# Kernel optimization log

Measured on AMD Instinct MI355X. Metric: run time of the kernel, lower is better.

The kernel has to match this reference:

```python
import jax, jax.numpy as jnp
import numpy as np

BATCH, SEQ, D_MODEL, N_HEADS, D_HEAD = 2, 2048, 2048, 16, 128
ATTN_SCALE = np.sqrt(D_HEAD).astype(np.float32)
IGNORE = jnp.float32(-1e5)


def setup_inputs() -> dict:
    key = jax.random.key(0)
    ks = jax.random.split(key, 5)
    init = 1.0 / np.sqrt(D_MODEL)
    return {
        "x": jax.random.normal(ks[0], (BATCH, SEQ, D_MODEL), jnp.float32),
        "W_Q": jax.random.normal(ks[1], (N_HEADS, D_MODEL, D_HEAD), jnp.float32) * init,
        "W_K": jax.random.normal(ks[2], (N_HEADS, D_MODEL, D_HEAD), jnp.float32) * init,
        "W_V": jax.random.normal(ks[3], (N_HEADS, D_MODEL, D_HEAD), jnp.float32) * init,
        "W_O": jax.random.normal(ks[4], (N_HEADS, D_HEAD, D_MODEL), jnp.float32) * init,
        "b_Q": jnp.zeros((N_HEADS, D_HEAD), jnp.float32),
        "b_K": jnp.zeros((N_HEADS, D_HEAD), jnp.float32),
        "b_V": jnp.zeros((N_HEADS, D_HEAD), jnp.float32),
        "b_O": jnp.zeros((D_MODEL,), jnp.float32),
    }


def reference(x, W_Q, W_K, W_V, W_O, b_Q, b_K, b_V, b_O):
    # q,k,v: [batch, pos, head, d_head]
    q = jnp.einsum('bpd,hde->bphe', x, W_Q) + b_Q
    k = jnp.einsum('bpd,hde->bphe', x, W_K) + b_K
    v = jnp.einsum('bpd,hde->bphe', x, W_V) + b_V
    # scores: [batch, head, query_pos, key_pos]
    scores = jnp.einsum('bqhe,bkhe->bhqk', q, k) / ATTN_SCALE
    S = x.shape[1]
    causal = jnp.tril(jnp.ones((S, S), bool))
    scores = jnp.where(causal, scores, IGNORE)
    attn = jax.nn.softmax(scores, axis=-1)
    z = jnp.einsum('bkhe,bhqk->bqhe', v, attn)
    out = jnp.einsum('bqhe,hed->bqd', z, W_O) + b_O
    return out
```

## Files before the change

### kernel.cpp

```cpp
#include <hip/hip_runtime.h>

typedef unsigned int uint;
typedef unsigned short ushort;
typedef __bf16 bf16x8 __attribute__((ext_vector_type(8)));
typedef float f32x4 __attribute__((ext_vector_type(4)));
typedef uint u32x4 __attribute__((ext_vector_type(4)));

#define DEV static __device__ __forceinline__

#define BATCH 2
#define SEQ 2048
#define DMODEL 2048
#define NHEADS 16
#define DHEAD 128
#define MROWS (BATCH*SEQ)
#define RSCALE 0.08838834764831845f
#define LOG2E  1.4426950408889634f

DEV float fast_exp2(float x) { return __builtin_amdgcn_exp2f(x); }

DEV bf16x8 as_frag(u32x4 v) { return __builtin_bit_cast(bf16x8, v); }
DEV ushort f2bf(float f) {
  uint u = __builtin_bit_cast(uint, f);
  u += 0x7fffu + ((u >> 16) & 1u);
  return (ushort)(u >> 16);
}
DEV u32x4 lds_ld16(const ushort* p) { return *(const u32x4*)p; }

DEV void async_cp16(const ushort* g, ushort* l) {
  __builtin_amdgcn_global_load_lds(
      (const __attribute__((address_space(1))) uint*)g,
      (__attribute__((address_space(3))) uint*)l, 16, 0, 0);
}

__global__ __launch_bounds__(256) void prep(
    const float* __restrict__ x,
    const float* __restrict__ Wq, const float* __restrict__ Wk,
    const float* __restrict__ Wv, const float* __restrict__ Wo,
    ushort* __restrict__ xb, ushort* __restrict__ WqT,
    ushort* __restrict__ WkT, ushort* __restrict__ WvT,
    ushort* __restrict__ WoT)
{
  int id = blockIdx.x;
  if (id < 8192) {
    int i = id * 256 + threadIdx.x;
    float4 v = ((const float4*)x)[i];
    union { ushort u[4]; uint2 w; } o;
    o.u[0] = f2bf(v.x); o.u[1] = f2bf(v.y); o.u[2] = f2bf(v.z); o.u[3] = f2bf(v.w);
    ((uint2*)xb)[i] = o.w;
    return;
  }
  __shared__ ushort t[32][33];
  id -= 8192;
  const float* src; ushort* dst; int R, C, c0, r0;
  if (id < 12288) {
    int which = id >> 12;
    int r = id & 4095;
    int slice = r >> 8;
    int rem = r & 255;
    int ty = rem >> 2, tx = rem & 3;
    const float* S[3] = {Wq, Wk, Wv};
    ushort* D[3] = {WqT, WkT, WvT};
    src = S[which] + (size_t)slice * DMODEL * DHEAD;
    dst = D[which] + (size_t)slice * DMODEL * DHEAD;
    R = DMODEL; C = DHEAD; c0 = tx * 32; r0 = ty * 32;
  } else {
    id -= 12288;
    int tx = id & 63, ty = id >> 6;
    src = Wo; dst = WoT; R = DMODEL; C = DMODEL; c0 = tx * 32; r0 = ty * 32;
  }
  int xx = threadIdx.x & 31, yy = threadIdx.x >> 5;
  #pragma unroll
  for (int i = 0; i < 32; i += 8)
    t[yy + i][xx] = f2bf(src[(size_t)(r0 + yy + i) * C + (c0 + xx)]);
  __syncthreads();
  #pragma unroll
  for (int i = 0; i < 32; i += 8)
    dst[(size_t)(c0 + yy + i) * R + (r0 + xx)] = t[xx][yy + i];
}

__global__ __launch_bounds__(256, 4) void gemm_qkv(
    const ushort* __restrict__ xb,
    const ushort* __restrict__ WqT, const ushort* __restrict__ WkT,
    const ushort* __restrict__ WvT,
    const float* __restrict__ bQ, const float* __restrict__ bK,
    const float* __restrict__ bV,
    ushort* __restrict__ Qo, ushort* __restrict__ Ko, ushort* __restrict__ Vt)
{
  int mt = blockIdx.x;
  int h  = blockIdx.y;
  int which = blockIdx.z;
  const ushort* Bt = (which == 0) ? WqT : (which == 1) ? WkT : WvT;
  const float* bias = (which == 0) ? bQ : (which == 1) ? bK : bV;
  Bt += (size_t)h * DHEAD * DMODEL;
  bias += h * DHEAD;

  __shared__ __align__(16) ushort As[128 * 64];
  __shared__ __align__(16) ushort Bs[128 * 64];

  int tid = threadIdx.x, lane = tid & 63, w = tid >> 6;
  int wm = w >> 1, wn = w & 1;
  int l16 = lane & 15, quad = lane >> 4;

  const ushort* Ag = xb + (size_t)(mt * 128) * DMODEL;

  int soff[4]; int sc[4];
  #pragma unroll
  for (int t = 0; t < 4; t++) {
    int c = w * 4 + t;
    int r = c * 8 + (lane >> 3);
    int p = lane & 7;
    int g = p ^ (r & 7);
    soff[t] = r * DMODEL + g * 8;
    sc[t] = c * 512;
  }

  f32x4 acc[4][4] = {};

  for (int k0 = 0; k0 < DMODEL; k0 += 64) {
    __syncthreads();
    #pragma unroll
    for (int t = 0; t < 4; t++) {
      async_cp16(Ag + soff[t] + k0, As + sc[t]);
      async_cp16(Bt + soff[t] + k0, Bs + sc[t]);
    }
    __syncthreads();
    #pragma unroll
    for (int kk = 0; kk < 2; kk++) {
      bf16x8 a[4], b[4];
      #pragma unroll
      for (int i = 0; i < 4; i++) {
        int row = wm * 64 + i * 16 + l16;
        int p = (kk * 4 + quad) ^ (l16 & 7);
        a[i] = as_frag(lds_ld16(As + row * 64 + p * 8));
      }
      #pragma unroll
      for (int i = 0; i < 4; i++) {
        int row = wn * 64 + i * 16 + l16;
        int p = (kk * 4 + quad) ^ (l16 & 7);
        b[i] = as_frag(lds_ld16(Bs + row * 64 + p * 8));
      }
      #pragma unroll
      for (int i = 0; i < 4; i++)
        #pragma unroll
        for (int j = 0; j < 4; j++)
          acc[i][j] = __builtin_amdgcn_mfma_f32_16x16x32_bf16(a[i], b[j], acc[i][j], 0, 0, 0);
    }
  }

  float scale = (which == 0) ? RSCALE * LOG2E : 1.0f;
  #pragma unroll
  for (int i = 0; i < 4; i++) {
    #pragma unroll
    for (int j = 0; j < 4; j++) {
      int col = wn * 64 + j * 16 + l16;
      float bb = bias[col];
      #pragma unroll
      for (int r = 0; r < 4; r++) {
        int row = mt * 128 + wm * 64 + i * 16 + quad * 4 + r;
        int b_ = row >> 11, p = row & 2047;
        int bh = b_ * NHEADS + h;
        ushort val = f2bf((acc[i][j][r] + bb) * scale);
        if (which == 2) {
          Vt[((size_t)bh * DHEAD + col) * SEQ + p] = val;
        } else {
          ushort* Out = (which == 0) ? Qo : Ko;
          Out[((size_t)bh * SEQ + p) * DHEAD + col] = val;
        }
      }
    }
  }
}

__global__ __launch_bounds__(256, 2) void flash_attn(
    const ushort* __restrict__ Q, const ushort* __restrict__ K,
    const ushort* __restrict__ Vt, ushort* __restrict__ Z)
{
  int a  = blockIdx.x;
  int bh = blockIdx.y;
  const ushort* Qg = Q + (size_t)bh * SEQ * DHEAD;
  const ushort* Kg = K + (size_t)bh * SEQ * DHEAD;
  const ushort* Vg = Vt + (size_t)bh * DHEAD * SEQ;

  __shared__ __align__(16) ushort Ks[2][64 * 128];
  __shared__ __align__(16) ushort Vs[2][128 * 64];
  __shared__ __align__(16) ushort Ps[64 * 72];

  int tid = threadIdx.x, lane = tid & 63, w = tid >> 6;
  int l16 = lane & 15, quad = lane >> 4;

  int kOff[4], vOff[4], cLds[4];
  #pragma unroll
  for (int t = 0; t < 4; t++) {
    int c = w * 4 + t;
    cLds[t] = c * 512;
    int rk = c * 4 + (lane >> 4);
    int pk = lane & 15;
    int gk = (pk & 8) | ((pk & 7) ^ (rk & 7));
    kOff[t] = rk * DHEAD + gk * 8;
    int ev = c * 8 + (lane >> 3);
    int pv = lane & 7;
    int gv = pv ^ (ev & 7);
    vOff[t] = ev * SEQ + gv * 8;
  }

  #pragma unroll
  for (int ph = 0; ph < 2; ph++) {
    int qt = ph ? a : (31 - a);
    int q0 = qt * 64;

    bf16x8 qf[4];
    int qrow = q0 + w * 16 + l16;
    #pragma unroll
    for (int kb = 0; kb < 4; kb++)
      qf[kb] = as_frag(*(const u32x4*)(Qg + qrow * DHEAD + kb * 32 + quad * 8));

    float m_i[4], l_i[4];
    #pragma unroll
    for (int i = 0; i < 4; i++) { m_i[i] = -1e30f; l_i[i] = 0.0f; }
    f32x4 zacc[8] = {};

    #pragma unroll
    for (int t = 0; t < 4; t++) {
      async_cp16(Kg + kOff[t], Ks[0] + cLds[t]);
      async_cp16(Vg + vOff[t], Vs[0] + cLds[t]);
    }
    __syncthreads();

    for (int j = 0; j <= qt; j++) {
      int cur = j & 1;
      if (j < qt) {
        int k1 = (j + 1) * 64;
        #pragma unroll
        for (int t = 0; t < 4; t++) {
          async_cp16(Kg + k1 * DHEAD + kOff[t], Ks[cur ^ 1] + cLds[t]);
          async_cp16(Vg + k1 + vOff[t], Vs[cur ^ 1] + cLds[t]);
        }
      }
      const ushort* KsC = Ks[cur];
      const ushort* VsC = Vs[cur];

      f32x4 s[4] = {};
      #pragma unroll
      for (int kb = 0; kb < 4; kb++) {
        #pragma unroll
        for (int n = 0; n < 4; n++) {
          int r = n * 16 + l16;
          int ug = kb * 4 + quad;
          int p = (ug & 8) | ((ug & 7) ^ (r & 7));
          bf16x8 b = as_frag(lds_ld16(KsC + r * 128 + p * 8));
          s[n] = __builtin_amdgcn_mfma_f32_16x16x32_bf16(qf[kb], b, s[n], 0, 0, 0);
        }
      }
      if (j == qt) {
        #pragma unroll
        for (int n = 0; n < 4; n++)
          #pragma unroll
          for (int i = 0; i < 4; i++) {
            int qr = 16 * w + quad * 4 + i;
            int kr = n * 16 + l16;
            if (kr > qr) s[n][i] = -1e30f;
          }
      }
      float mx[4];
      #pragma unroll
      for (int i = 0; i < 4; i++)
        mx[i] = fmaxf(fmaxf(s[0][i], s[1][i]), fmaxf(s[2][i], s[3][i]));
      #pragma unroll
      for (int off = 1; off < 16; off <<= 1)
        #pragma unroll
        for (int i = 0; i < 4; i++)
          mx[i] = fmaxf(mx[i], __shfl_xor(mx[i], off, 64));

      float alpha[4], rsum[4];
      #pragma unroll
      for (int i = 0; i < 4; i++) {
        float mn = fmaxf(m_i[i], mx[i]);
        alpha[i] = fast_exp2(m_i[i] - mn);
        m_i[i] = mn;
        rsum[i] = 0.0f;
      }
      #pragma unroll
      for (int n = 0; n < 4; n++)
        #pragma unroll
        for (int i = 0; i < 4; i++) {
          float p = fast_exp2(s[n][i] - m_i[i]);
          rsum[i] += p;
          int row = 16 * w + quad * 4 + i, col = n * 16 + l16;
          Ps[row * 72 + col] = f2bf(p);
        }
      #pragma unroll
      for (int off = 1; off < 16; off <<= 1)
        #pragma unroll
        for (int i = 0; i < 4; i++)
          rsum[i] += __shfl_xor(rsum[i], off, 64);
      #pragma unroll
      for (int i = 0; i < 4; i++) l_i[i] = l_i[i] * alpha[i] + rsum[i];
      #pragma unroll
      for (int n = 0; n < 8; n++)
        #pragma unroll
        for (int i = 0; i < 4; i++) zacc[n][i] *= alpha[i];

      #pragma unroll
      for (int kk = 0; kk < 2; kk++) {
        bf16x8 af = as_frag(lds_ld16(Ps + (w * 16 + l16) * 72 + (kk * 4 + quad) * 8));
        #pragma unroll
        for (int n = 0; n < 8; n++) {
          int e = n * 16 + l16;
          int ug = kk * 4 + quad;
          int p = ug ^ (e & 7);
          bf16x8 b = as_frag(lds_ld16(VsC + e * 64 + p * 8));
          zacc[n] = __builtin_amdgcn_mfma_f32_16x16x32_bf16(af, b, zacc[n], 0, 0, 0);
        }
      }
      __syncthreads();
    }

    int b_ = bh >> 4, h = bh & 15;
    #pragma unroll
    for (int n = 0; n < 8; n++)
      #pragma unroll
      for (int i = 0; i < 4; i++) {
        int row = q0 + 16 * w + quad * 4 + i;
        int col = h * DHEAD + n * 16 + l16;
        Z[((size_t)(b_ * SEQ + row)) * DMODEL + col] = f2bf(zacc[n][i] / l_i[i]);
      }
  }
}

__global__ __launch_bounds__(256, 4) void gemm_out(
    const ushort* __restrict__ Zin, const ushort* __restrict__ WoT,
    const float* __restrict__ bO, float* __restrict__ out)
{
  int mt = blockIdx.x, ntile = blockIdx.y;
  __shared__ __align__(16) ushort As[128 * 64];
  __shared__ __align__(16) ushort Bs[128 * 64];
  int tid = threadIdx.x, lane = tid & 63, w = tid >> 6;
  int wm = w >> 1, wn = w & 1;
  int l16 = lane & 15, quad = lane >> 4;

  const ushort* Ag = Zin + (size_t)(mt * 128) * DMODEL;
  const ushort* Bg = WoT + (size_t)(ntile * 128) * DMODEL;

  int soff[4]; int sc[4];
  #pragma unroll
  for (int t = 0; t < 4; t++) {
    int c = w * 4 + t;
    int r = c * 8 + (lane >> 3);
    int p = lane & 7;
    int g = p ^ (r & 7);
    soff[t] = r * DMODEL + g * 8;
    sc[t] = c * 512;
  }

  f32x4 acc[4][4] = {};
  for (int k0 = 0; k0 < DMODEL; k0 += 64) {
    __syncthreads();
    #pragma unroll
    for (int t = 0; t < 4; t++) {
      async_cp16(Ag + soff[t] + k0, As + sc[t]);
      async_cp16(Bg + soff[t] + k0, Bs + sc[t]);
    }
    __syncthreads();
    #pragma unroll
    for (int kk = 0; kk < 2; kk++) {
      bf16x8 a[4], b[4];
      #pragma unroll
      for (int i = 0; i < 4; i++) {
        int row = wm * 64 + i * 16 + l16;
        int p = (kk * 4 + quad) ^ (l16 & 7);
        a[i] = as_frag(lds_ld16(As + row * 64 + p * 8));
      }
      #pragma unroll
      for (int i = 0; i < 4; i++) {
        int row = wn * 64 + i * 16 + l16;
        int p = (kk * 4 + quad) ^ (l16 & 7);
        b[i] = as_frag(lds_ld16(Bs + row * 64 + p * 8));
      }
      #pragma unroll
      for (int i = 0; i < 4; i++)
        #pragma unroll
        for (int j = 0; j < 4; j++)
          acc[i][j] = __builtin_amdgcn_mfma_f32_16x16x32_bf16(a[i], b[j], acc[i][j], 0, 0, 0);
    }
  }
  #pragma unroll
  for (int i = 0; i < 4; i++) {
    #pragma unroll
    for (int j = 0; j < 4; j++) {
      int col = ntile * 128 + wn * 64 + j * 16 + l16;
      float bb = bO[col];
      #pragma unroll
      for (int r = 0; r < 4; r++) {
        int row = mt * 128 + wm * 64 + i * 16 + quad * 4 + r;
        out[(size_t)row * DMODEL + col] = acc[i][j][r] + bb;
      }
    }
  }
}

extern "C" void kernel_launch(void* const* d_in, const int* in_sizes, int n_in,
                              void* d_out, int out_size, void* d_ws, size_t ws_size,
                              hipStream_t stream)
{
  const float* x  = (const float*)d_in[0];
  const float* Wq = (const float*)d_in[1];
  const float* Wk = (const float*)d_in[2];
  const float* Wv = (const float*)d_in[3];
  const float* Wo = (const float*)d_in[4];
  const float* bQ = (const float*)d_in[5];
  const float* bK = (const float*)d_in[6];
  const float* bV = (const float*)d_in[7];
  const float* bO = (const float*)d_in[8];
  float* out = (float*)d_out;

  ushort* ws = (ushort*)d_ws;
  const size_t WSZ = (size_t)NHEADS * DHEAD * DMODEL;
  const size_t QSZ = (size_t)BATCH * NHEADS * SEQ * DHEAD;
  ushort* xb  = ws;
  ushort* WqT = xb + (size_t)MROWS * DMODEL;
  ushort* WkT = WqT + WSZ;
  ushort* WvT = WkT + WSZ;
  ushort* WoT = WvT + WSZ;
  ushort* Qb  = WoT + (size_t)DMODEL * DMODEL;
  ushort* Kb  = Qb + QSZ;
  ushort* VtB = Kb + QSZ;
  ushort* Zb  = VtB + QSZ;

  dim3 tb(256);
  prep<<<dim3(24576), tb, 0, stream>>>(x, Wq, Wk, Wv, Wo,
                                       xb, WqT, WkT, WvT, WoT);

  gemm_qkv<<<dim3(32, 16, 3), tb, 0, stream>>>(xb, WqT, WkT, WvT, bQ, bK, bV,
                                               Qb, Kb, VtB);

  flash_attn<<<dim3(16, 32), tb, 0, stream>>>(Qb, Kb, VtB, Zb);

  gemm_out<<<dim3(32, 16), tb, 0, stream>>>(Zb, WoT, bO, out);
}
```

Measured before the change: 375.9 us.

## Rewrite QKV GEMM with 256x256 tiles, 8 waves, and double-buffered async pipeline

The QKV projection GEMM moves from 128x128 tiles with 4 waves and a load-sync-compute loop to 256x256 tiles with 8 waves. The new loop double-buffers half-K slices in LDS, prefetches several stages ahead with explicit vmcnt waits, and raises wave priority around the MFMA bursts. A remapped 1D grid groups blocks across the Q/K/V panels, with a head-spanning epilogue. The aim is to hide global load latency and raise reuse per LDS byte, at the cost of more LDS, more registers and fragile hand-tuned wait counts.

```diff
diff --git a/kernel.cpp b/kernel.cpp
--- a/kernel.cpp
+++ b/kernel.cpp
@@ -79,7 +79,7 @@
     dst[(size_t)(c0 + yy + i) * R + (r0 + xx)] = t[xx][yy + i];
 }
 
-__global__ __launch_bounds__(256, 4) void gemm_qkv(
+__global__ __launch_bounds__(512, 2) void gemm_qkv(
     const ushort* __restrict__ xb,
     const ushort* __restrict__ WqT, const ushort* __restrict__ WkT,
     const ushort* __restrict__ WvT,
@@ -87,85 +87,154 @@
     const float* __restrict__ bV,
     ushort* __restrict__ Qo, ushort* __restrict__ Ko, ushort* __restrict__ Vt)
 {
-  int mt = blockIdx.x;
-  int h  = blockIdx.y;
-  int which = blockIdx.z;
-  const ushort* Bt = (which == 0) ? WqT : (which == 1) ? WkT : WvT;
+  int id = blockIdx.x;
+  int W = (id & 7) * 48 + (id >> 3);
+  int which = W >> 7;
+  int rem = W & 127;
+  int nt = rem >> 4;
+  int mt = rem & 15;
+
+  const ushort* Bpan = (which == 0) ? WqT : (which == 1) ? WkT : WvT;
   const float* bias = (which == 0) ? bQ : (which == 1) ? bK : bV;
-  Bt += (size_t)h * DHEAD * DMODEL;
-  bias += h * DHEAD;
-
-  __shared__ __align__(16) ushort As[128 * 64];
-  __shared__ __align__(16) ushort Bs[128 * 64];
+  const ushort* Ag = xb + (size_t)(mt * 256) * DMODEL;
+  const ushort* Bt = Bpan + (size_t)(nt * 256) * DMODEL;
+
+  __shared__ __align__(16) ushort As[2 * 2 * 256 * 32];
+  __shared__ __align__(16) ushort Bs[2 * 2 * 256 * 32];
 
   int tid = threadIdx.x, lane = tid & 63, w = tid >> 6;
-  int wm = w >> 1, wn = w & 1;
+  int wm = w >> 2, wn = w & 3;
   int l16 = lane & 15, quad = lane >> 4;
-
-  const ushort* Ag = xb + (size_t)(mt * 128) * DMODEL;
-
-  int soff[4]; int sc[4];
-  #pragma unroll
-  for (int t = 0; t < 4; t++) {
-    int c = w * 4 + t;
-    int r = c * 8 + (lane >> 3);
-    int p = lane & 7;
-    int g = p ^ (r & 7);
-    soff[t] = r * DMODEL + g * 8;
-    sc[t] = c * 512;
-  }
-
-  f32x4 acc[4][4] = {};
-
-  for (int k0 = 0; k0 < DMODEL; k0 += 64) {
-    __syncthreads();
-    #pragma unroll
-    for (int t = 0; t < 4; t++) {
-      async_cp16(Ag + soff[t] + k0, As + sc[t]);
-      async_cp16(Bt + soff[t] + k0, Bs + sc[t]);
-    }
-    __syncthreads();
-    #pragma unroll
-    for (int kk = 0; kk < 2; kk++) {
-      bf16x8 a[4], b[4];
-      #pragma unroll
-      for (int i = 0; i < 4; i++) {
-        int row = wm * 64 + i * 16 + l16;
-        int p = (kk * 4 + quad) ^ (l16 & 7);
-        a[i] = as_frag(lds_ld16(As + row * 64 + p * 8));
-      }
-      #pragma unroll
-      for (int i = 0; i < 4; i++) {
-        int row = wn * 64 + i * 16 + l16;
-        int p = (kk * 4 + quad) ^ (l16 & 7);
-        b[i] = as_frag(lds_ld16(Bs + row * 64 + p * 8));
-      }
-      #pragma unroll
-      for (int i = 0; i < 4; i++)
-        #pragma unroll
-        for (int j = 0; j < 4; j++)
-          acc[i][j] = __builtin_amdgcn_mfma_f32_16x16x32_bf16(a[i], b[j], acc[i][j], 0, 0, 0);
-    }
+  int sg8 = (quad ^ ((l16 >> 1) & 3)) * 8;
+
+  int lbase0 = (w * 64) * 8;
+  int lbase1 = (512 + w * 64) * 8;
+  int gof0, gof1;
+  {
+    int s0 = w * 64 + lane, s1 = 512 + w * 64 + lane;
+    int r0 = s0 >> 2, r1 = s1 >> 2;
+    int g0 = (s0 & 3) ^ ((r0 >> 1) & 3);
+    int g1 = (s1 & 3) ^ ((r1 >> 1) & 3);
+    gof0 = r0 * DMODEL + g0 * 8;
+    gof1 = r1 * DMODEL + g1 * 8;
+  }
+
+  auto stage = [&](int j) {
+    if (j >= 128) return;
+    int ts = j >> 2, h2 = j & 3, hk = h2 >> 1;
+    const ushort* G; ushort* L;
+    if (h2 & 1) { G = Bt; L = Bs; } else { G = Ag; L = As; }
+    L += (((ts & 1) << 1) | hk) * (256 * 32);
+    G += (size_t)ts * 64 + hk * 32;
+    async_cp16(G + gof0, L + lbase0);
+    async_cp16(G + gof1, L + lbase1);
+  };
+
+  f32x4 acc[8][4] = {};
+  bf16x8 Af[4], Bf[4];
+
+  stage(0); stage(1); stage(2); stage(3);
+  asm volatile("s_waitcnt vmcnt(4)" ::: "memory");
+  stage(4); stage(5); stage(6);
+  asm volatile("s_waitcnt vmcnt(6)" ::: "memory");
+  __builtin_amdgcn_s_barrier();
+
+  for (int t = 0; t < 32; ++t) {
+    int buf = t & 1;
+    const ushort* A0 = As + ((buf << 1) | 0) * (256 * 32);
+    const ushort* A1 = As + ((buf << 1) | 1) * (256 * 32);
+    const ushort* B0 = Bs + ((buf << 1) | 0) * (256 * 32);
+    const ushort* B1 = Bs + ((buf << 1) | 1) * (256 * 32);
+    int j0 = 4 * t + 7;
+
+    #pragma unroll
+    for (int n = 0; n < 4; n++)
+      Bf[n] = as_frag(lds_ld16(B0 + (wn * 64 + n * 16 + l16) * 32 + sg8));
+    #pragma unroll
+    for (int i = 0; i < 4; i++)
+      Af[i] = as_frag(lds_ld16(A0 + (wm * 128 + i * 16 + l16) * 32 + sg8));
+    stage(j0);
+    __builtin_amdgcn_s_barrier();
+    asm volatile("s_waitcnt lgkmcnt(0)" ::: "memory");
+    __builtin_amdgcn_s_setprio(1);
+    #pragma unroll
+    for (int i = 0; i < 4; i++)
+      #pragma unroll
+      for (int n = 0; n < 4; n++)
+        acc[i][n] = __builtin_amdgcn_mfma_f32_16x16x32_bf16(Af[i], Bf[n], acc[i][n], 0, 0, 0);
+    __builtin_amdgcn_s_setprio(0);
+    __builtin_amdgcn_s_barrier();
+
+    #pragma unroll
+    for (int i = 0; i < 4; i++)
+      Af[i] = as_frag(lds_ld16(A0 + (wm * 128 + 64 + i * 16 + l16) * 32 + sg8));
+    stage(j0 + 1);
+    __builtin_amdgcn_s_barrier();
+    asm volatile("s_waitcnt lgkmcnt(0)" ::: "memory");
+    __builtin_amdgcn_s_setprio(1);
+    #pragma unroll
+    for (int i = 0; i < 4; i++)
+      #pragma unroll
+      for (int n = 0; n < 4; n++)
+        acc[4 + i][n] = __builtin_amdgcn_mfma_f32_16x16x32_bf16(Af[i], Bf[n], acc[4 + i][n], 0, 0, 0);
+    __builtin_amdgcn_s_setprio(0);
+    __builtin_amdgcn_s_barrier();
+
+    #pragma unroll
+    for (int n = 0; n < 4; n++)
+      Bf[n] = as_frag(lds_ld16(B1 + (wn * 64 + n * 16 + l16) * 32 + sg8));
+    #pragma unroll
+    for (int i = 0; i < 4; i++)
+      Af[i] = as_frag(lds_ld16(A1 + (wm * 128 + i * 16 + l16) * 32 + sg8));
+    stage(j0 + 2);
+    __builtin_amdgcn_s_barrier();
+    asm volatile("s_waitcnt lgkmcnt(0)" ::: "memory");
+    __builtin_amdgcn_s_setprio(1);
+    #pragma unroll
+    for (int i = 0; i < 4; i++)
+      #pragma unroll
+      for (int n = 0; n < 4; n++)
+        acc[i][n] = __builtin_amdgcn_mfma_f32_16x16x32_bf16(Af[i], Bf[n], acc[i][n], 0, 0, 0);
+    __builtin_amdgcn_s_setprio(0);
+    __builtin_amdgcn_s_barrier();
+
+    #pragma unroll
+    for (int i = 0; i < 4; i++)
+      Af[i] = as_frag(lds_ld16(A1 + (wm * 128 + 64 + i * 16 + l16) * 32 + sg8));
+    stage(j0 + 3);
+    __builtin_amdgcn_s_barrier();
+    asm volatile("s_waitcnt lgkmcnt(0)" ::: "memory");
+    __builtin_amdgcn_s_setprio(1);
+    #pragma unroll
+    for (int i = 0; i < 4; i++)
+      #pragma unroll
+      for (int n = 0; n < 4; n++)
+        acc[4 + i][n] = __builtin_amdgcn_mfma_f32_16x16x32_bf16(Af[i], Bf[n], acc[4 + i][n], 0, 0, 0);
+    __builtin_amdgcn_s_setprio(0);
+    if (t < 30)      asm volatile("s_waitcnt vmcnt(6)" ::: "memory");
+    else if (t == 30) asm volatile("s_waitcnt vmcnt(0)" ::: "memory");
+    __builtin_amdgcn_s_barrier();
   }
 
   float scale = (which == 0) ? RSCALE * LOG2E : 1.0f;
   #pragma unroll
-  for (int i = 0; i < 4; i++) {
-    #pragma unroll
-    for (int j = 0; j < 4; j++) {
-      int col = wn * 64 + j * 16 + l16;
+  for (int mi = 0; mi < 8; mi++) {
+    #pragma unroll
+    for (int n = 0; n < 4; n++) {
+      int col = nt * 256 + wn * 64 + n * 16 + l16;
+      int h = col >> 7, e = col & 127;
       float bb = bias[col];
       #pragma unroll
       for (int r = 0; r < 4; r++) {
-        int row = mt * 128 + wm * 64 + i * 16 + quad * 4 + r;
+        int row = mt * 256 + wm * 128 + mi * 16 + quad * 4 + r;
         int b_ = row >> 11, p = row & 2047;
         int bh = b_ * NHEADS + h;
-        ushort val = f2bf((acc[i][j][r] + bb) * scale);
+        ushort val = f2bf((acc[mi][n][r] + bb) * scale);
         if (which == 2) {
-          Vt[((size_t)bh * DHEAD + col) * SEQ + p] = val;
+          Vt[((size_t)bh * DHEAD + e) * SEQ + p] = val;
         } else {
           ushort* Out = (which == 0) ? Qo : Ko;
-          Out[((size_t)bh * SEQ + p) * DHEAD + col] = val;
+          Out[((size_t)bh * SEQ + p) * DHEAD + e] = val;
         }
       }
     }
@@ -427,14 +496,13 @@
   ushort* VtB = Kb + QSZ;
   ushort* Zb  = VtB + QSZ;
 
-  dim3 tb(256);
-  prep<<<dim3(24576), tb, 0, stream>>>(x, Wq, Wk, Wv, Wo,
-                                       xb, WqT, WkT, WvT, WoT);
-
-  gemm_qkv<<<dim3(32, 16, 3), tb, 0, stream>>>(xb, WqT, WkT, WvT, bQ, bK, bV,
-                                               Qb, Kb, VtB);
-
-  flash_attn<<<dim3(16, 32), tb, 0, stream>>>(Qb, Kb, VtB, Zb);
-
-  gemm_out<<<dim3(32, 16), tb, 0, stream>>>(Zb, WoT, bO, out);
-}
+  prep<<<dim3(24576), dim3(256), 0, stream>>>(x, Wq, Wk, Wv, Wo,
+                                              xb, WqT, WkT, WvT, WoT);
+
+  gemm_qkv<<<dim3(384), dim3(512), 0, stream>>>(xb, WqT, WkT, WvT, bQ, bK, bV,
+                                                Qb, Kb, VtB);
+
+  flash_attn<<<dim3(16, 32), dim3(256), 0, stream>>>(Qb, Kb, VtB, Zb);
+
+  gemm_out<<<dim3(32, 16), dim3(256), 0, stream>>>(Zb, WoT, bO, out);
+}
```

Result: slower. 446.5 us (+18.8%).
